# Kernel optimization log

Hardware: AMD Instinct MI355X
Metric: run time of the kernel (lower is better)

## Reference

```python
import jax, jax.numpy as jnp
import numpy as np


def setup_inputs() -> dict:
    key = jax.random.key(0)
    kW, kH, kT = jax.random.split(key, 3)
    N, rank, M = 1024, 8, 4096
    W = jax.random.normal(kW, (N, rank), dtype=jnp.float32)
    H = jax.random.normal(kH, (rank, M), dtype=jnp.float32)
    tau = jax.random.normal(kT, (N, rank), dtype=jnp.float32)
    return {"W": W, "H": H, "tau": tau}


def reference(W, H, tau):
    # W: [N, rank] float, H: [rank, M] float, tau: [N, rank] float
    M = H.shape[1]
    Nf = M // 2 + 1
    # FFT of nonneg-constrained H, keep first Nf bins, rebuild full Hermitian spectrum
    Hf = jnp.fft.fft(jax.nn.softplus(H), axis=1)[:, :Nf]            # [rank, Nf]
    Hf_rev = Hf[:, 1:Nf - 1][:, ::-1]                               # [rank, M - Nf]
    Hft = jnp.concatenate([Hf, jnp.conj(Hf_rev)], axis=1)           # [rank, M]
    f = jnp.arange(M, dtype=jnp.float32) / M                        # [M]
    # phase shift per (sample, component, freq): omega = exp(-i 2 pi tau f)
    omega = jnp.exp((-2j * jnp.pi) * (tau[:, :, None] * f))         # [N, rank, M] complex64
    Wp = jax.nn.softplus(W).astype(omega.dtype)                     # [N, rank]
    # fused: V[N,M] = sum_d softplus(W)[N,d] * omega[N,d,M] * Hft[d,M]
    V = jnp.einsum('Nd,NdM,dM->NM', Wp, omega, Hft)
    return V
```

## Files before the change

kernel.cpp:

```cpp
#include <hip/hip_runtime.h>
#include <math.h>

#define N_ROWS 1024
#define RANK   8
#define M_COLS 4096

#define R_ROWS   2
#define T_PTS    4
#define M_STRIDE 512

__device__ float  g_Wp [N_ROWS * RANK];
__device__ float2 g_Hft[RANK * M_COLS];

__device__ __forceinline__ float softplus_f(float x) {
    float t = __expf(x);
    float r = 0.69314718056f * __log2f(1.0f + t);
    return (x > 20.0f) ? x : r;
}
__device__ __forceinline__ float sin_rev(float x) { return __builtin_amdgcn_sinf(x); }
__device__ __forceinline__ float cos_rev(float x) { return __builtin_amdgcn_cosf(x); }
__device__ __forceinline__ float fract_f(float x) { return __builtin_amdgcn_fractf(x); }
__device__ __forceinline__ float rfl(float x) {
    return __int_as_float(__builtin_amdgcn_readfirstlane(__float_as_int(x)));
}

__global__ void fft_fused(const float* __restrict__ H,
                          const float* __restrict__ W) {
    __shared__ float  sHs[M_COLS];
    __shared__ float2 sY[4 * 64];

    int tid = threadIdx.x;
    int d   = blockIdx.x >> 4;
    int m0b = (blockIdx.x & 15) << 2;

    if (blockIdx.x < 32) {
        int t = blockIdx.x * 256 + tid;
        g_Wp[t] = softplus_f(W[t]);
    }

    const float4* Hrow4 = (const float4*)(H + d * M_COLS);
    #pragma unroll
    for (int p = 0; p < 4; ++p) {
        int i = p * 256 + tid;
        float4 h4 = Hrow4[i];
        sHs[i*4+0] = softplus_f(h4.x);
        sHs[i*4+1] = softplus_f(h4.y);
        sHs[i*4+2] = softplus_f(h4.z);
        sHs[i*4+3] = softplus_f(h4.w);
    }
    __syncthreads();

    {
        int k0 = tid & 63, j = tid >> 6;
        int m0 = m0b + j;
        float mrev = (float)m0 * (1.0f / 64.0f);
        float rr =  cos_rev(mrev);
        float ri = -sin_rev(mrev);
        float twr = 1.0f, twi = 0.0f;
        float ar = 0.0f, ai = 0.0f;
        #pragma unroll
        for (int k1 = 0; k1 < 64; ++k1) {
            float v = sHs[(k1 << 6) + k0];
            ar = fmaf(v, twr, ar);
            ai = fmaf(v, twi, ai);
            float nr = fmaf(twr, rr, -(twi * ri));
            twi      = fmaf(twr, ri,   twi * rr);
            twr = nr;
        }
        sY[(j << 6) + k0] = make_float2(ar, ai);
    }
    __syncthreads();

    {
        int m1 = tid & 63, j = tid >> 6;
        int m  = (m1 << 6) + m0b + j;
        float mrev = (float)m * (1.0f / 4096.0f);
        float rr =  cos_rev(mrev);
        float ri = -sin_rev(mrev);
        float twr = 1.0f, twi = 0.0f;
        float ar = 0.0f, ai = 0.0f;
        #pragma unroll
        for (int k0 = 0; k0 < 64; ++k0) {
            float2 y = sY[(j << 6) + k0];
            ar = fmaf(y.x, twr, fmaf(-y.y, twi, ar));
            ai = fmaf(y.x, twi, fmaf( y.y, twr, ai));
            float nr = fmaf(twr, rr, -(twi * ri));
            twi      = fmaf(twr, ri,   twi * rr);
            twr = nr;
        }
        g_Hft[d * M_COLS + m] = make_float2(ar, ai);
    }
}

__global__ void shiftnmf_main(const float* __restrict__ tau,
                              float* __restrict__ out) {
    int tid = threadIdx.x;
    int m0  = blockIdx.x * 256 + tid;
    int n0  = blockIdx.y * R_ROWS;

    float fm0 = (float)(1 + m0) * (1.0f / (float)M_COLS);

    float accm[R_ROWS][T_PTS];
    float accx[R_ROWS][T_PTS];
    #pragma unroll
    for (int r = 0; r < R_ROWS; ++r)
        #pragma unroll
        for (int j = 0; j < T_PTS; ++j) { accm[r][j] = 0.0f; accx[r][j] = 0.0f; }

    #pragma unroll
    for (int d = 0; d < RANK; ++d) {
        float ur[R_ROWS], ui[R_ROWS];
        float vrs[R_ROWS], vis[R_ROWS];
        float ws[R_ROWS], wcr[R_ROWS], wci[R_ROWS];
        #pragma unroll
        for (int r = 0; r < R_ROWS; ++r) {
            int n    = n0 + r;
            float w  = g_Wp[n * RANK + d];
            float tv = tau [n * RANK + d];
            ws[r] = rfl(w);
            float rv = fract_f(tv * 0.125f);
            vrs[r] = rfl(cos_rev(rv));
            vis[r] = rfl(sin_rev(rv));
            float rc = fract_f(-tv);
            float cr = cos_rev(rc), ci = sin_rev(rc);
            wcr[r] = rfl(w * cr);
            wci[r] = rfl(w * ci);
            float r0 = fract_f(tv * fm0);
            ur[r] = cos_rev(r0);
            ui[r] = sin_rev(r0);
        }

        const float2* hp = g_Hft + d * M_COLS + 1 + m0;
        #pragma unroll
        for (int j = 0; j < T_PTS; ++j) {
            float2 h = hp[j * M_STRIDE];
            #pragma unroll
            for (int r = 0; r < R_ROWS; ++r) {
                float t1 = ui[r] * h.y;
                float zr = fmaf(ur[r], h.x, t1);
                float t2 = ui[r] * h.x;
                float zi = fmaf(ur[r], h.y, -t2);
                accm[r][j] = fmaf(ws[r],  zr, accm[r][j]);
                accx[r][j] = fmaf(wcr[r], zr, fmaf(wci[r], zi, accx[r][j]));
                if (j < T_PTS - 1) {
                    float nr = fmaf(ur[r], vrs[r], -(ui[r] * vis[r]));
                    ui[r]    = fmaf(ur[r], vis[r],   ui[r] * vrs[r]);
                    ur[r]    = nr;
                }
            }
        }
    }

    #pragma unroll
    for (int r = 0; r < R_ROWS; ++r) {
        float* op = out + (n0 + r) * M_COLS;
        #pragma unroll
        for (int j = 0; j < T_PTS; ++j)
            op[1 + m0 + j * M_STRIDE] = accm[r][j];
        #pragma unroll
        for (int j = 0; j < T_PTS; ++j)
            op[4095 - m0 - j * M_STRIDE] = accx[r][j];
    }

    if (blockIdx.x == 0 && tid == 0) {
        #pragma unroll
        for (int r = 0; r < R_ROWS; ++r) {
            int n = n0 + r;
            float a = 0.0f;
            #pragma unroll
            for (int d = 0; d < RANK; ++d)
                a = fmaf(g_Wp[n * RANK + d], g_Hft[d * M_COLS].x, a);
            out[n * M_COLS] = a;
        }
    }
}

extern "C" void kernel_launch(void* const* d_in, const int* in_sizes, int n_in,
                              void* d_out, int out_size, void* d_ws, size_t ws_size,
                              hipStream_t stream) {
    const float* W   = (const float*)d_in[0];
    const float* H   = (const float*)d_in[1];
    const float* tau = (const float*)d_in[2];

    fft_fused<<<dim3(RANK * 16), dim3(256), 0, stream>>>(H, W);

    dim3 grid(2, N_ROWS / R_ROWS);
    shiftnmf_main<<<grid, dim3(256), 0, stream>>>(tau, (float*)d_out);
}
```

Baseline: 20.20 us.

## Precompute per-(n,d) twiddle tables in FFT kernel and halve points per thread

Moves the per-(n,d) softplus, phase-step and conjugate-weight trig computations into the first kernel, storing them in float4/float2 global tables, so the main kernel only loads them rather than recomputing them redundantly in every block. Points per thread drop from 4 to 2 with the stride doubled to 1024, which doubles the grid in the M dimension for more parallelism. In exchange there is extra global table traffic and more per-block setup amortised over fewer outputs.

```diff
diff --git a/kernel.cpp b/kernel.cpp
--- a/kernel.cpp
+++ b/kernel.cpp
@@ -6,11 +6,12 @@
 #define M_COLS 4096
 
 #define R_ROWS   2
-#define T_PTS    4
-#define M_STRIDE 512
+#define T_PTS    2
+#define M_STRIDE 1024
 
-__device__ float  g_Wp [N_ROWS * RANK];
 __device__ float2 g_Hft[RANK * M_COLS];
+__device__ float4 g_Tab4[N_ROWS * RANK];
+__device__ float2 g_Tab2[N_ROWS * RANK];
 
 __device__ __forceinline__ float softplus_f(float x) {
     float t = __expf(x);
@@ -25,7 +26,8 @@
 }
 
 __global__ void fft_fused(const float* __restrict__ H,
-                          const float* __restrict__ W) {
+                          const float* __restrict__ W,
+                          const float* __restrict__ tau) {
     __shared__ float  sHs[M_COLS];
     __shared__ float2 sY[4 * 64];
 
@@ -35,7 +37,17 @@
 
     if (blockIdx.x < 32) {
         int t = blockIdx.x * 256 + tid;
-        g_Wp[t] = softplus_f(W[t]);
+        float w  = softplus_f(W[t]);
+        float tv = tau[t];
+        float rv = fract_f(tv * ((float)M_STRIDE / (float)M_COLS));
+        float4 t4;
+        t4.x = cos_rev(rv);
+        t4.y = sin_rev(rv);
+        float rc = fract_f(-tv);
+        t4.z = w * cos_rev(rc);
+        t4.w = w * sin_rev(rc);
+        g_Tab4[t] = t4;
+        g_Tab2[t] = make_float2(w, tv);
     }
 
     const float4* Hrow4 = (const float4*)(H + d * M_COLS);
@@ -92,8 +104,7 @@
     }
 }
 
-__global__ void shiftnmf_main(const float* __restrict__ tau,
-                              float* __restrict__ out) {
+__global__ void shiftnmf_main(float* __restrict__ out) {
     int tid = threadIdx.x;
     int m0  = blockIdx.x * 256 + tid;
     int n0  = blockIdx.y * R_ROWS;
@@ -110,21 +121,17 @@
     #pragma unroll
     for (int d = 0; d < RANK; ++d) {
         float ur[R_ROWS], ui[R_ROWS];
-        float vrs[R_ROWS], vis[R_ROWS];
+        float vr[R_ROWS], vi[R_ROWS];
         float ws[R_ROWS], wcr[R_ROWS], wci[R_ROWS];
         #pragma unroll
         for (int r = 0; r < R_ROWS; ++r) {
-            int n    = n0 + r;
-            float w  = g_Wp[n * RANK + d];
-            float tv = tau [n * RANK + d];
-            ws[r] = rfl(w);
-            float rv = fract_f(tv * 0.125f);
-            vrs[r] = rfl(cos_rev(rv));
-            vis[r] = rfl(sin_rev(rv));
-            float rc = fract_f(-tv);
-            float cr = cos_rev(rc), ci = sin_rev(rc);
-            wcr[r] = rfl(w * cr);
-            wci[r] = rfl(w * ci);
+            int nd = (n0 + r) * RANK + d;
+            float4 t4 = g_Tab4[nd];
+            float2 t2 = g_Tab2[nd];
+            vr[r]  = rfl(t4.x);  vi[r]  = rfl(t4.y);
+            wcr[r] = rfl(t4.z);  wci[r] = rfl(t4.w);
+            ws[r]  = rfl(t2.x);
+            float tv = rfl(t2.y);
             float r0 = fract_f(tv * fm0);
             ur[r] = cos_rev(r0);
             ui[r] = sin_rev(r0);
@@ -138,13 +145,13 @@
             for (int r = 0; r < R_ROWS; ++r) {
                 float t1 = ui[r] * h.y;
                 float zr = fmaf(ur[r], h.x, t1);
-                float t2 = ui[r] * h.x;
-                float zi = fmaf(ur[r], h.y, -t2);
+                float t2v = ui[r] * h.x;
+                float zi = fmaf(ur[r], h.y, -t2v);
                 accm[r][j] = fmaf(ws[r],  zr, accm[r][j]);
                 accx[r][j] = fmaf(wcr[r], zr, fmaf(wci[r], zi, accx[r][j]));
                 if (j < T_PTS - 1) {
-                    float nr = fmaf(ur[r], vrs[r], -(ui[r] * vis[r]));
-                    ui[r]    = fmaf(ur[r], vis[r],   ui[r] * vrs[r]);
+                    float nr = fmaf(ur[r], vr[r], -(ui[r] * vi[r]));
+                    ui[r]    = fmaf(ur[r], vi[r],   ui[r] * vr[r]);
                     ur[r]    = nr;
                 }
             }
@@ -169,7 +176,7 @@
             float a = 0.0f;
             #pragma unroll
             for (int d = 0; d < RANK; ++d)
-                a = fmaf(g_Wp[n * RANK + d], g_Hft[d * M_COLS].x, a);
+                a = fmaf(g_Tab2[n * RANK + d].x, g_Hft[d * M_COLS].x, a);
             out[n * M_COLS] = a;
         }
     }
@@ -182,8 +189,8 @@
     const float* H   = (const float*)d_in[1];
     const float* tau = (const float*)d_in[2];
 
-    fft_fused<<<dim3(RANK * 16), dim3(256), 0, stream>>>(H, W);
+    fft_fused<<<dim3(RANK * 16), dim3(256), 0, stream>>>(H, W, tau);
 
-    dim3 grid(2, N_ROWS / R_ROWS);
-    shiftnmf_main<<<grid, dim3(256), 0, stream>>>(tau, (float*)d_out);
+    dim3 grid(M_COLS / 2 / (256 * T_PTS), N_ROWS / R_ROWS);
+    shiftnmf_main<<<grid, dim3(256), 0, stream>>>((float*)d_out);
 }
```

After: 19.20 us. -4.9%, faster.
